# Kernel optimization log

Measured on AMD Instinct MI355X. Metric: run time of the kernel, lower is better.

The kernel has to match this reference:

```python
import jax, jax.numpy as jnp
import numpy as np

B, T, E, H, V, O = 64, 512, 128, 256, 100000, 1


def setup_inputs() -> dict:
    key = jax.random.key(0)
    ks = jax.random.split(key, 10)
    sE, sH = 1.0 / np.sqrt(E), 1.0 / np.sqrt(H)
    return {
        "x": jax.random.randint(ks[0], (B, T), 0, V),
        "emb_table": jax.random.normal(ks[1], (V, E), jnp.float32) * 0.1,
        "W_ih": jax.random.normal(ks[2], (4 * H, E), jnp.float32) * sE,  # torch gate order i,f,g,o
        "W_hh": jax.random.normal(ks[3], (4 * H, H), jnp.float32) * sH,
        "b_ih": jnp.zeros((4 * H,), jnp.float32),  # biases init'd to 0 in source
        "b_hh": jnp.zeros((4 * H,), jnp.float32),
        "Wm": jax.random.normal(ks[4], (H, H), jnp.float32) * sH,
        "bm": jnp.zeros((H,), jnp.float32),
        "Wf": jax.random.normal(ks[5], (O, H), jnp.float32) * sH,
        "bf": jnp.zeros((O,), jnp.float32),
    }


def reference(x, emb_table, W_ih, W_hh, b_ih, b_hh, Wm, bm, Wf, bf):
    batch = x.shape[0]
    hid = W_hh.shape[1]
    # vectorized replacement for the per-(i,j) python-loop embedding copy
    embeds = emb_table[x]                                  # [B,T,E]
    # precompute input contribution to all gates for every timestep
    gx = jnp.einsum('bte,ge->btg', embeds, W_ih) + b_ih     # [B,T,4H]
    gx = jnp.swapaxes(gx, 0, 1)                             # [T,B,4H]
    h0 = jnp.zeros((batch, hid), embeds.dtype)
    c0 = jnp.zeros((batch, hid), embeds.dtype)

    def step(carry, g_t):
        h, c = carry
        g = g_t + h @ W_hh.T + b_hh                         # [B,4H]
        i, f, gg, o = jnp.split(g, 4, axis=-1)
        i, f, o = jax.nn.sigmoid(i), jax.nn.sigmoid(f), jax.nn.sigmoid(o)
        c = f * c + i * jnp.tanh(gg)
        h = o * jnp.tanh(c)
        return (h, c), h

    (hT, cT), hs = jax.lax.scan(step, (h0, c0), gx)
    out = jnp.swapaxes(hs, 0, 1)                            # [B,T,H]
    out = out @ Wm.T + bm                                   # ffmiddle
    out = out @ Wf.T + bf                                   # fc -> [B,T,O]
    sig_out = jax.nn.sigmoid(out).reshape(batch, -1).mean(axis=1)  # [B]
    # hidden = (h_n, c_n) with leading num_layers=1 dim, as in torch
    return sig_out, hT[None, :, :], cT[None, :, :]
```

## Files before the change

kernel.cpp:

```cpp
#include <hip/hip_runtime.h>


#define BATCH 64
#define TSTEPS 512
#define EDIM 128
#define HDIM 256
#define G4H 1024

typedef short bf16x8 __attribute__((ext_vector_type(8)));
typedef short bf16x4 __attribute__((ext_vector_type(4)));
typedef float f32x4 __attribute__((ext_vector_type(4)));

__device__ __forceinline__ unsigned short f2bf(float f) {
  unsigned u = __builtin_bit_cast(unsigned, f);
  return (unsigned short)((u + 0x7fffu + ((u >> 16) & 1u)) >> 16);
}
__device__ __forceinline__ float bf2f(unsigned short h) {
  unsigned u = ((unsigned)h) << 16;
  return __builtin_bit_cast(float, u);
}
__device__ __forceinline__ unsigned pk2(float a, float b) {
  return (unsigned)f2bf(a) | ((unsigned)f2bf(b) << 16);
}
__device__ __forceinline__ float fsig(float x) {
  return __builtin_amdgcn_rcpf(1.f + __expf(-x));
}
__device__ __forceinline__ float ftanh(float x) {
  return 1.f - 2.f * __builtin_amdgcn_rcpf(__expf(2.f * x) + 1.f);
}
__device__ __forceinline__ bf16x8 ldfrag(const unsigned short* p) {
  bf16x4 a = *(const bf16x4*)p;
  bf16x4 b = *(const bf16x4*)(p + 16);
  return __builtin_shufflevector(a, b, 0, 1, 2, 3, 4, 5, 6, 7);
}
__device__ __forceinline__ bf16x8 pack8(float4 v0, float4 v1) {
  bf16x8 f;
  f[0] = (short)f2bf(v0.x); f[1] = (short)f2bf(v0.y);
  f[2] = (short)f2bf(v0.z); f[3] = (short)f2bf(v0.w);
  f[4] = (short)f2bf(v1.x); f[5] = (short)f2bf(v1.y);
  f[6] = (short)f2bf(v1.z); f[7] = (short)f2bf(v1.w);
  return f;
}

__global__ __launch_bounds__(256) void k_gx(const int* __restrict__ x,
                                            const float* __restrict__ emb,
                                            const float* __restrict__ Wih,
                                            const float* __restrict__ bih,
                                            unsigned short* __restrict__ gx3) {
  const int t = blockIdx.x;
  const int g0 = blockIdx.y * 64;
  const int tid = threadIdx.x;
  __shared__ unsigned short Al[64 * 136];
  __shared__ unsigned short Bl[64 * 136];
  __shared__ int tok[64];
  if (tid < 64) tok[tid] = x[tid * TSTEPS + t];
  __syncthreads();
  {
    const int r = tid >> 2, c0 = (tid & 3) * 32;
    const float* asrc = emb + (size_t)tok[r] * EDIM + c0;
    const float* bsrc = Wih + (size_t)(g0 + r) * EDIM + c0;
#pragma unroll
    for (int s = 0; s < 32; s += 8) {
      float4 a0 = *(const float4*)(asrc + s);
      float4 a1 = *(const float4*)(asrc + s + 4);
      uint4 pa = {pk2(a0.x, a0.y), pk2(a0.z, a0.w), pk2(a1.x, a1.y), pk2(a1.z, a1.w)};
      *(uint4*)&Al[r * 136 + c0 + s] = pa;
      float4 b0 = *(const float4*)(bsrc + s);
      float4 b1 = *(const float4*)(bsrc + s + 4);
      uint4 pb = {pk2(b0.x, b0.y), pk2(b0.z, b0.w), pk2(b1.x, b1.y), pk2(b1.z, b1.w)};
      *(uint4*)&Bl[r * 136 + c0 + s] = pb;
    }
  }
  __syncthreads();
  const int lane = tid & 63, w = tid >> 6;
  const int lo = lane & 15, hi = lane >> 4;
  const int mb = (w & 1) * 32, nb = (w >> 1) * 32;
  f32x4 acc[2][2];
#pragma unroll
  for (int jj = 0; jj < 2; ++jj) {
    float bv = bih[g0 + nb + jj * 16 + lo];
    acc[0][jj] = (f32x4){bv, bv, bv, bv};
    acc[1][jj] = acc[0][jj];
  }
#pragma unroll
  for (int kk = 0; kk < 4; ++kk) {
    bf16x8 af0 = ldfrag(&Al[(mb + lo) * 136 + kk * 32 + hi * 4]);
    bf16x8 af1 = ldfrag(&Al[(mb + 16 + lo) * 136 + kk * 32 + hi * 4]);
    bf16x8 bf0 = ldfrag(&Bl[(nb + lo) * 136 + kk * 32 + hi * 4]);
    bf16x8 bf1 = ldfrag(&Bl[(nb + 16 + lo) * 136 + kk * 32 + hi * 4]);
    acc[0][0] = __builtin_amdgcn_mfma_f32_16x16x32_bf16(af0, bf0, acc[0][0], 0, 0, 0);
    acc[0][1] = __builtin_amdgcn_mfma_f32_16x16x32_bf16(af0, bf1, acc[0][1], 0, 0, 0);
    acc[1][0] = __builtin_amdgcn_mfma_f32_16x16x32_bf16(af1, bf0, acc[1][0], 0, 0, 0);
    acc[1][1] = __builtin_amdgcn_mfma_f32_16x16x32_bf16(af1, bf1, acc[1][1], 0, 0, 0);
  }
#pragma unroll
  for (int i = 0; i < 2; ++i)
#pragma unroll
    for (int jj = 0; jj < 2; ++jj) {
      int grp = (w & 1) * 2 + i;
      int col = g0 + nb + jj * 16 + lo;
      int g = col >> 8, jc = col & 255;
      int halfb = jc >> 7, wv = (jc >> 4) & 7, lov = jc & 15;
      size_t base = (((size_t)(t * 8 + grp * 2 + halfb) * 8 + wv) * 64 +
                     (hi * 16 + lov)) * 16 + g * 4;
      unsigned long long val =
          (unsigned long long)pk2(acc[i][jj][0], acc[i][jj][1]) |
          ((unsigned long long)pk2(acc[i][jj][2], acc[i][jj][3]) << 32);
      *(unsigned long long*)&gx3[base] = val;
    }
}

__global__ __launch_bounds__(512, 2) void k_rec(const unsigned short* __restrict__ gx3,
                                                const float* __restrict__ Whh,
                                                const float* __restrict__ bhh,
                                                const float* __restrict__ weff,
                                                unsigned long long* __restrict__ hx,
                                                float* __restrict__ out) {
  const int tid = threadIdx.x;
  const int bp = blockIdx.x;
  const int grp = bp >> 1, half = bp & 1;
  const int b0 = grp * 16;
  const int lane = tid & 63, w = tid >> 6;
  const int lo = lane & 15, hi = lane >> 4;
  const int j = half * 128 + w * 16 + lo;
  __shared__ unsigned short h_lds[2][32 * 136];
  bf16x8 wf[4][8];
  float bhv[4];
#pragma unroll
  for (int g = 0; g < 4; ++g) {
    const float* wr = Whh + (size_t)(g * 256 + j) * HDIM;
    bhv[g] = bhh[g * 256 + j];
#pragma unroll
    for (int kk = 0; kk < 8; ++kk) {
      const float* p = wr + kk * 32 + hi * 8;
      wf[g][kk] = pack8(*(const float4*)p, *(const float4*)(p + 4));
    }
  }
  const int hb_b = tid >> 5, hb_g = tid & 31;
  float wv8[8];
#pragma unroll
  for (int e = 0; e < 8; ++e) wv8[e] = weff[hb_g * 8 + e];
  const float c0 = weff[256];
  float sig_acc = 0.f;
  for (int i = tid; i < 32 * 136 / 2; i += 512) ((unsigned*)h_lds[0])[i] = 0u;
  const unsigned short* gp = gx3 + (((size_t)bp * 8 + w) * 64 + lane) * 16;
  unsigned gwE[8], gwO[8];
  {
    uint4 a = *(const uint4*)(gp);
    uint4 b = *(const uint4*)(gp + 8);
    gwE[0] = a.x; gwE[1] = a.y; gwE[2] = a.z; gwE[3] = a.w;
    gwE[4] = b.x; gwE[5] = b.y; gwE[6] = b.z; gwE[7] = b.w;
    uint4 c2 = *(const uint4*)(gp + 65536);
    uint4 d2 = *(const uint4*)(gp + 65536 + 8);
    gwO[0] = c2.x; gwO[1] = c2.y; gwO[2] = c2.z; gwO[3] = c2.w;
    gwO[4] = d2.x; gwO[5] = d2.y; gwO[6] = d2.z; gwO[7] = d2.w;
  }
  float c[4] = {0.f, 0.f, 0.f, 0.f};
  float hv[4];
  f32x4 acc[4];
  const int ob = (j >> 3) * 136 + (j & 7);
  const int jp = ((half ^ 1) * 128) + ((tid >> 6) << 4) + (tid & 15);
  const int hip = (tid >> 4) & 3;
  const int pb = (jp >> 3) * 136 + (jp & 7);
  __syncthreads();

  auto cinit = [&](const unsigned (&G)[8]) {
#pragma unroll
    for (int g = 0; g < 4; ++g)
#pragma unroll
      for (int r = 0; r < 4; ++r) {
        unsigned word = G[g * 2 + (r >> 1)];
        unsigned short v = (r & 1) ? (unsigned short)(word >> 16) : (unsigned short)word;
        acc[g][r] = bf2f(v) + bhv[g];
      }
  };
  auto mfma_own = [&](int buf) {
    if (half == 0) {
#pragma unroll
      for (int kk = 0; kk < 4; ++kk) {
        bf16x8 a = *(const bf16x8*)&h_lds[buf][(kk * 4 + hi) * 136 + lo * 8];
#pragma unroll
        for (int g = 0; g < 4; ++g)
          acc[g] = __builtin_amdgcn_mfma_f32_16x16x32_bf16(a, wf[g][kk], acc[g], 0, 0, 0);
      }
    } else {
#pragma unroll
      for (int kk = 4; kk < 8; ++kk) {
        bf16x8 a = *(const bf16x8*)&h_lds[buf][(kk * 4 + hi) * 136 + lo * 8];
#pragma unroll
        for (int g = 0; g < 4; ++g)
          acc[g] = __builtin_amdgcn_mfma_f32_16x16x32_bf16(a, wf[g][kk], acc[g], 0, 0, 0);
      }
    }
  };
  auto mfma_par = [&](int buf) {
    if (half == 0) {
#pragma unroll
      for (int kk = 4; kk < 8; ++kk) {
        bf16x8 a = *(const bf16x8*)&h_lds[buf][(kk * 4 + hi) * 136 + lo * 8];
#pragma unroll
        for (int g = 0; g < 4; ++g)
          acc[g] = __builtin_amdgcn_mfma_f32_16x16x32_bf16(a, wf[g][kk], acc[g], 0, 0, 0);
      }
    } else {
#pragma unroll
      for (int kk = 0; kk < 4; ++kk) {
        bf16x8 a = *(const bf16x8*)&h_lds[buf][(kk * 4 + hi) * 136 + lo * 8];
#pragma unroll
        for (int g = 0; g < 4; ++g)
          acc[g] = __builtin_amdgcn_mfma_f32_16x16x32_bf16(a, wf[g][kk], acc[g], 0, 0, 0);
      }
    }
  };
  auto update_store = [&](int t) {
    const unsigned wt = (unsigned)(t + 1);
    unsigned short hbf[4];
#pragma unroll
    for (int r = 0; r < 4; ++r) {
      float iv = fsig(acc[0][r]), fv = fsig(acc[1][r]);
      float gv = ftanh(acc[2][r]), ov = fsig(acc[3][r]);
      c[r] = fv * c[r] + iv * gv;
      hv[r] = ov * ftanh(c[r]);
      hbf[r] = f2bf(hv[r]);
    }
    const int par = (int)(wt & 1u);
    unsigned long long* dst = &hx[((size_t)(par * 8 + bp)) * 1024 + w * 128 + lane * 2];
    const unsigned long long tg = ((unsigned long long)wt) << 32;
    __hip_atomic_store(&dst[0], tg | (unsigned long long)pk2(hv[0], hv[1]),
                       __ATOMIC_RELAXED, __HIP_MEMORY_SCOPE_AGENT);
    __hip_atomic_store(&dst[1], tg | (unsigned long long)pk2(hv[2], hv[3]),
                       __ATOMIC_RELAXED, __HIP_MEMORY_SCOPE_AGENT);
    asm volatile("" ::: "memory");
#pragma unroll
    for (int r = 0; r < 4; ++r) h_lds[par][ob + (hi * 4 + r) * 8] = hbf[r];
  };
  auto head = [&](int buf) {
    bf16x8 hh = *(const bf16x8*)&h_lds[buf][hb_g * 136 + hb_b * 8];
    float s = 0.f;
#pragma unroll
    for (int e = 0; e < 8; ++e) s += bf2f((unsigned short)hh[e]) * wv8[e];
    s += __shfl_xor(s, 1);  s += __shfl_xor(s, 2);  s += __shfl_xor(s, 4);
    s += __shfl_xor(s, 8);  s += __shfl_xor(s, 16);
    sig_acc += fsig(s + c0);
  };
  auto gx_issue = [&](int s, unsigned (&G)[8]) {
    const unsigned short* q = gp + (size_t)s * 65536;
    uint4 a = *(const uint4*)(q);
    uint4 b = *(const uint4*)(q + 8);
    G[0] = a.x; G[1] = a.y; G[2] = a.z; G[3] = a.w;
    G[4] = b.x; G[5] = b.y; G[6] = b.z; G[7] = b.w;
  };
  auto poll_write = [&](int t) {
    const unsigned wt = (unsigned)(t + 1);
    const int par = (int)(wt & 1u);
    unsigned long long* src = &hx[((size_t)(par * 8 + (bp ^ 1))) * 1024 + tid * 2];
    unsigned long long a0 = __hip_atomic_load(&src[0], __ATOMIC_RELAXED, __HIP_MEMORY_SCOPE_AGENT);
    unsigned long long a1 = __hip_atomic_load(&src[1], __ATOMIC_RELAXED, __HIP_MEMORY_SCOPE_AGENT);
    unsigned long long b0 = __hip_atomic_load(&src[0], __ATOMIC_RELAXED, __HIP_MEMORY_SCOPE_AGENT);
    unsigned long long b1 = __hip_atomic_load(&src[1], __ATOMIC_RELAXED, __HIP_MEMORY_SCOPE_AGENT);
    unsigned long long v0, v1;
    for (;;) {
      if ((unsigned)(a0 >> 32) == wt && (unsigned)(a1 >> 32) == wt) { v0 = a0; v1 = a1; break; }
      a0 = b0; a1 = b1;
      b0 = __hip_atomic_load(&src[0], __ATOMIC_RELAXED, __HIP_MEMORY_SCOPE_AGENT);
      b1 = __hip_atomic_load(&src[1], __ATOMIC_RELAXED, __HIP_MEMORY_SCOPE_AGENT);
    }
    h_lds[par][pb + (hip * 4 + 0) * 8] = (unsigned short)v0;
    h_lds[par][pb + (hip * 4 + 1) * 8] = (unsigned short)(v0 >> 16);
    h_lds[par][pb + (hip * 4 + 2) * 8] = (unsigned short)v1;
    h_lds[par][pb + (hip * 4 + 3) * 8] = (unsigned short)(v1 >> 16);
  };
  auto body = [&](int t, unsigned (&Gc)[8], unsigned (&Gf)[8]) {
    mfma_par(t & 1);
    update_store(t);
    if (t + 2 < TSTEPS) gx_issue(t + 2, Gf);
    __syncthreads();
    if (t < TSTEPS - 1) {
      cinit(Gc);
      mfma_own((t + 1) & 1);
    }
    head(t & 1);
    poll_write(t);
    __syncthreads();
  };

  cinit(gwE);
  update_store(0);
  gx_issue(2, gwE);
  __syncthreads();
  cinit(gwO);
  mfma_own(1);
  poll_write(0);
  __syncthreads();
  for (int t = 1; t + 1 < TSTEPS - 1; t += 2) {
    body(t, gwE, gwO);
    body(t + 1, gwO, gwE);
  }
  body(TSTEPS - 1, gwE, gwO);
  head(0);
  if (half == 0 && hb_g == 0) out[b0 + hb_b] = sig_acc * (1.f / 512.f);
#pragma unroll
  for (int r = 0; r < 4; ++r) {
    const int b = b0 + hi * 4 + r;
    out[64 + b * HDIM + j] = hv[r];
    out[64 + BATCH * HDIM + b * HDIM + j] = c[r];
  }
}

__global__ __launch_bounds__(256) void k_weff(const float* __restrict__ Wm,
                                              const float* __restrict__ bm,
                                              const float* __restrict__ Wf,
                                              const float* __restrict__ bfb,
                                              float* __restrict__ weff) {
  const int k = threadIdx.x;
  __shared__ float red[256];
  float acc = 0.f;
#pragma unroll 8
  for (int jj = 0; jj < 256; ++jj) acc += Wf[jj] * Wm[jj * 256 + k];
  weff[k] = acc;
  red[k] = bm[k] * Wf[k];
  __syncthreads();
  for (int s = 128; s > 0; s >>= 1) {
    if (k < s) red[k] += red[k + s];
    __syncthreads();
  }
  if (k == 0) weff[256] = red[0] + bfb[0];
}

extern "C" void kernel_launch(void* const* d_in, const int* in_sizes, int n_in,
                              void* d_out, int out_size, void* d_ws, size_t ws_size,
                              hipStream_t stream) {
  (void)in_sizes; (void)n_in; (void)out_size; (void)ws_size;
  const int* x = (const int*)d_in[0];
  const float* emb = (const float*)d_in[1];
  const float* Wih = (const float*)d_in[2];
  const float* Whh = (const float*)d_in[3];
  const float* bih = (const float*)d_in[4];
  const float* bhh = (const float*)d_in[5];
  const float* Wm  = (const float*)d_in[6];
  const float* bm  = (const float*)d_in[7];
  const float* Wf  = (const float*)d_in[8];
  const float* bf  = (const float*)d_in[9];
  float* out = (float*)d_out;
  char* ws = (char*)d_ws;
  const size_t gx_bytes = (size_t)TSTEPS * BATCH * G4H * 2;
  const size_t hx_bytes = (size_t)2 * 8 * 1024 * 8;
  unsigned short* gx3 = (unsigned short*)ws;
  unsigned long long* hx = (unsigned long long*)(ws + gx_bytes);
  float* weff = (float*)(ws + gx_bytes + hx_bytes);
  hipMemsetAsync(hx, 0, hx_bytes, stream);
  k_gx<<<dim3(512, 16), 256, 0, stream>>>(x, emb, Wih, bih, gx3);
  k_weff<<<1, 256, 0, stream>>>(Wm, bm, Wf, bf, weff);
  k_rec<<<8, 512, 0, stream>>>(gx3, Whh, bhh, weff, hx, out);
}
```

Baseline: 1.034 ms.

## Split exchange roles across warps and overlap peer polling with MFMA

Cross-block hidden-state exchange now uses a role split: warps 0-3 read packed h from LDS and publish it to global with four 64-bit tagged stores each, while warps 4-7 issue the peer loads before their own-half MFMAs and only spin and write to LDS afterward. The gx prefetch is also moved to the start of each step. The aim is to hide the latency of cross-CU polling behind compute and to use wider, coalesced transfers. The cost is warp imbalance and an extra LDS read before publishing, which adds latency to the critical path.

```diff
diff --git a/kernel.cpp b/kernel.cpp
--- a/kernel.cpp
+++ b/kernel.cpp
@@ -159,9 +159,8 @@
   float hv[4];
   f32x4 acc[4];
   const int ob = (j >> 3) * 136 + (j & 7);
-  const int jp = ((half ^ 1) * 128) + ((tid >> 6) << 4) + (tid & 15);
-  const int hip = (tid >> 4) & 3;
-  const int pb = (jp >> 3) * 136 + (jp & 7);
+  const int ogran = half * 16;
+  const int pgran = (half ^ 1) * 16;
   __syncthreads();
 
   auto cinit = [&](const unsigned (&G)[8]) {
@@ -212,8 +211,8 @@
       }
     }
   };
-  auto update_store = [&](int t) {
-    const unsigned wt = (unsigned)(t + 1);
+  auto update = [&](int t) {
+    const int par = (int)((t + 1) & 1u);
     unsigned short hbf[4];
 #pragma unroll
     for (int r = 0; r < 4; ++r) {
@@ -223,14 +222,6 @@
       hv[r] = ov * ftanh(c[r]);
       hbf[r] = f2bf(hv[r]);
     }
-    const int par = (int)(wt & 1u);
-    unsigned long long* dst = &hx[((size_t)(par * 8 + bp)) * 1024 + w * 128 + lane * 2];
-    const unsigned long long tg = ((unsigned long long)wt) << 32;
-    __hip_atomic_store(&dst[0], tg | (unsigned long long)pk2(hv[0], hv[1]),
-                       __ATOMIC_RELAXED, __HIP_MEMORY_SCOPE_AGENT);
-    __hip_atomic_store(&dst[1], tg | (unsigned long long)pk2(hv[2], hv[3]),
-                       __ATOMIC_RELAXED, __HIP_MEMORY_SCOPE_AGENT);
-    asm volatile("" ::: "memory");
 #pragma unroll
     for (int r = 0; r < 4; ++r) h_lds[par][ob + (hi * 4 + r) * 8] = hbf[r];
   };
@@ -250,47 +241,84 @@
     G[0] = a.x; G[1] = a.y; G[2] = a.z; G[3] = a.w;
     G[4] = b.x; G[5] = b.y; G[6] = b.z; G[7] = b.w;
   };
-  auto poll_write = [&](int t) {
+  auto xstore = [&](int t) {
     const unsigned wt = (unsigned)(t + 1);
     const int par = (int)(wt & 1u);
-    unsigned long long* src = &hx[((size_t)(par * 8 + (bp ^ 1))) * 1024 + tid * 2];
-    unsigned long long a0 = __hip_atomic_load(&src[0], __ATOMIC_RELAXED, __HIP_MEMORY_SCOPE_AGENT);
-    unsigned long long a1 = __hip_atomic_load(&src[1], __ATOMIC_RELAXED, __HIP_MEMORY_SCOPE_AGENT);
-    unsigned long long b0 = __hip_atomic_load(&src[0], __ATOMIC_RELAXED, __HIP_MEMORY_SCOPE_AGENT);
-    unsigned long long b1 = __hip_atomic_load(&src[1], __ATOMIC_RELAXED, __HIP_MEMORY_SCOPE_AGENT);
-    unsigned long long v0, v1;
-    for (;;) {
-      if ((unsigned)(a0 >> 32) == wt && (unsigned)(a1 >> 32) == wt) { v0 = a0; v1 = a1; break; }
-      a0 = b0; a1 = b1;
-      b0 = __hip_atomic_load(&src[0], __ATOMIC_RELAXED, __HIP_MEMORY_SCOPE_AGENT);
-      b1 = __hip_atomic_load(&src[1], __ATOMIC_RELAXED, __HIP_MEMORY_SCOPE_AGENT);
-    }
-    h_lds[par][pb + (hip * 4 + 0) * 8] = (unsigned short)v0;
-    h_lds[par][pb + (hip * 4 + 1) * 8] = (unsigned short)(v0 >> 16);
-    h_lds[par][pb + (hip * 4 + 2) * 8] = (unsigned short)v1;
-    h_lds[par][pb + (hip * 4 + 3) * 8] = (unsigned short)(v1 >> 16);
+    const int b = tid >> 4, g = tid & 15;
+    uint4 hc = *(const uint4*)&h_lds[par][(ogran + g) * 136 + b * 8];
+    const unsigned long long tg = ((unsigned long long)wt) << 32;
+    unsigned long long* dst = &hx[((size_t)(par * 8 + bp)) * 1024];
+    __hip_atomic_store(&dst[0 * 256 + tid], tg | (unsigned long long)hc.x,
+                       __ATOMIC_RELAXED, __HIP_MEMORY_SCOPE_AGENT);
+    __hip_atomic_store(&dst[1 * 256 + tid], tg | (unsigned long long)hc.y,
+                       __ATOMIC_RELAXED, __HIP_MEMORY_SCOPE_AGENT);
+    __hip_atomic_store(&dst[2 * 256 + tid], tg | (unsigned long long)hc.z,
+                       __ATOMIC_RELAXED, __HIP_MEMORY_SCOPE_AGENT);
+    __hip_atomic_store(&dst[3 * 256 + tid], tg | (unsigned long long)hc.w,
+                       __ATOMIC_RELAXED, __HIP_MEMORY_SCOPE_AGENT);
+    asm volatile("" ::: "memory");
+  };
+  auto pissue = [&](int t, unsigned long long (&A)[4]) {
+    const unsigned wt = (unsigned)(t + 1);
+    const int par = (int)(wt & 1u);
+    const int pid = tid - 256;
+    const unsigned long long* src = &hx[((size_t)(par * 8 + (bp ^ 1))) * 1024];
+    A[0] = __hip_atomic_load(&src[0 * 256 + pid], __ATOMIC_RELAXED, __HIP_MEMORY_SCOPE_AGENT);
+    A[1] = __hip_atomic_load(&src[1 * 256 + pid], __ATOMIC_RELAXED, __HIP_MEMORY_SCOPE_AGENT);
+    A[2] = __hip_atomic_load(&src[2 * 256 + pid], __ATOMIC_RELAXED, __HIP_MEMORY_SCOPE_AGENT);
+    A[3] = __hip_atomic_load(&src[3 * 256 + pid], __ATOMIC_RELAXED, __HIP_MEMORY_SCOPE_AGENT);
+    asm volatile("" ::: "memory");
+  };
+  auto pfinish = [&](int t, unsigned long long (&A)[4]) {
+    const unsigned wt = (unsigned)(t + 1);
+    const int par = (int)(wt & 1u);
+    const int pid = tid - 256;
+    const unsigned long long* src = &hx[((size_t)(par * 8 + (bp ^ 1))) * 1024];
+    while (!((unsigned)(A[0] >> 32) == wt && (unsigned)(A[1] >> 32) == wt &&
+             (unsigned)(A[2] >> 32) == wt && (unsigned)(A[3] >> 32) == wt)) {
+      A[0] = __hip_atomic_load(&src[0 * 256 + pid], __ATOMIC_RELAXED, __HIP_MEMORY_SCOPE_AGENT);
+      A[1] = __hip_atomic_load(&src[1 * 256 + pid], __ATOMIC_RELAXED, __HIP_MEMORY_SCOPE_AGENT);
+      A[2] = __hip_atomic_load(&src[2 * 256 + pid], __ATOMIC_RELAXED, __HIP_MEMORY_SCOPE_AGENT);
+      A[3] = __hip_atomic_load(&src[3 * 256 + pid], __ATOMIC_RELAXED, __HIP_MEMORY_SCOPE_AGENT);
+    }
+    const int b = pid >> 4, g = pid & 15;
+    *(uint4*)&h_lds[par][(pgran + g) * 136 + b * 8] =
+        (uint4){(unsigned)A[0], (unsigned)A[1], (unsigned)A[2], (unsigned)A[3]};
   };
   auto body = [&](int t, unsigned (&Gc)[8], unsigned (&Gf)[8]) {
+    if (t + 2 < TSTEPS) gx_issue(t + 2, Gf);
     mfma_par(t & 1);
-    update_store(t);
-    if (t + 2 < TSTEPS) gx_issue(t + 2, Gf);
+    update(t);
     __syncthreads();
-    if (t < TSTEPS - 1) {
-      cinit(Gc);
-      mfma_own((t + 1) & 1);
-    }
-    head(t & 1);
-    poll_write(t);
+    if (w < 4) {
+      xstore(t);
+      if (t < TSTEPS - 1) { cinit(Gc); mfma_own((t + 1) & 1); }
+      head(t & 1);
+    } else {
+      unsigned long long A[4];
+      pissue(t, A);
+      if (t < TSTEPS - 1) { cinit(Gc); mfma_own((t + 1) & 1); }
+      head(t & 1);
+      pfinish(t, A);
+    }
     __syncthreads();
   };
 
   cinit(gwE);
-  update_store(0);
+  update(0);
   gx_issue(2, gwE);
   __syncthreads();
-  cinit(gwO);
-  mfma_own(1);
-  poll_write(0);
+  if (w < 4) {
+    xstore(0);
+    cinit(gwO);
+    mfma_own(1);
+  } else {
+    unsigned long long A[4];
+    pissue(0, A);
+    cinit(gwO);
+    mfma_own(1);
+    pfinish(0, A);
+  }
   __syncthreads();
   for (int t = 1; t + 1 < TSTEPS - 1; t += 2) {
     body(t, gwE, gwO);
```

Result: slower. 1.406 ms (+35.9%).

## Split recurrence across 16 blocks with fast sc0 polling and fallback exchange path

Applied to the files above, without the earlier changes.

The recurrent kernel now runs 16 blocks, each pair owning 8 batch rows instead of 16, with half-tiles padded in the MFMA rows. Hidden-state exchange between paired blocks is written twice: once with sc0 cache-hint inline-asm stores polled by a bounded spin loop, and once via agent-scope atomics used as a fallback when the fast path times out. The gx prefetch is also moved ahead of the MFMA phase. The aim is to cut per-step exchange latency and spread the work over more CUs, at the cost of duplicated stores, wasted MFMA rows and reliance on the cache-hint path being coherent enough.

```diff
diff --git a/kernel.cpp b/kernel.cpp
--- a/kernel.cpp
+++ b/kernel.cpp
@@ -110,16 +110,18 @@
     }
 }
 
-__global__ __launch_bounds__(512, 2) void k_rec(const unsigned short* __restrict__ gx3,
+__global__ __launch_bounds__(512, 1) void k_rec(const unsigned short* __restrict__ gx3,
                                                 const float* __restrict__ Whh,
                                                 const float* __restrict__ bhh,
                                                 const float* __restrict__ weff,
-                                                unsigned long long* __restrict__ hx,
+                                                unsigned long long* __restrict__ hxA,
+                                                unsigned long long* __restrict__ hxB,
                                                 float* __restrict__ out) {
   const int tid = threadIdx.x;
   const int bp = blockIdx.x;
-  const int grp = bp >> 1, half = bp & 1;
-  const int b0 = grp * 16;
+  const int grp = bp & 7, half = bp >> 3;
+  const int s = grp & 1;
+  const int slot = (grp >> 1) * 2 + half;
   const int lane = tid & 63, w = tid >> 6;
   const int lo = lane & 15, hi = lane >> 4;
   const int j = half * 128 + w * 16 + lo;
@@ -143,7 +145,8 @@
   const float c0 = weff[256];
   float sig_acc = 0.f;
   for (int i = tid; i < 32 * 136 / 2; i += 512) ((unsigned*)h_lds[0])[i] = 0u;
-  const unsigned short* gp = gx3 + (((size_t)bp * 8 + w) * 64 + lane) * 16;
+  const int glane = (s * 2 + (hi & 1)) * 16 + lo;
+  const unsigned short* gp = gx3 + (((size_t)slot * 8 + w) * 64 + glane) * 16;
   unsigned gwE[8], gwO[8];
   {
     uint4 a = *(const uint4*)(gp);
@@ -162,6 +165,7 @@
   const int jp = ((half ^ 1) * 128) + ((tid >> 6) << 4) + (tid & 15);
   const int hip = (tid >> 4) & 3;
   const int pb = (jp >> 3) * 136 + (jp & 7);
+  bool fast = true;
   __syncthreads();
 
   auto cinit = [&](const unsigned (&G)[8]) {
@@ -212,8 +216,8 @@
       }
     }
   };
-  auto update_store = [&](int t) {
-    const unsigned wt = (unsigned)(t + 1);
+  auto update = [&](int t) {
+    const int par = (int)((t + 1) & 1u);
     unsigned short hbf[4];
 #pragma unroll
     for (int r = 0; r < 4; ++r) {
@@ -223,74 +227,103 @@
       hv[r] = ov * ftanh(c[r]);
       hbf[r] = f2bf(hv[r]);
     }
-    const int par = (int)(wt & 1u);
-    unsigned long long* dst = &hx[((size_t)(par * 8 + bp)) * 1024 + w * 128 + lane * 2];
+    const unsigned wt = (unsigned)(t + 1);
     const unsigned long long tg = ((unsigned long long)wt) << 32;
-    __hip_atomic_store(&dst[0], tg | (unsigned long long)pk2(hv[0], hv[1]),
-                       __ATOMIC_RELAXED, __HIP_MEMORY_SCOPE_AGENT);
-    __hip_atomic_store(&dst[1], tg | (unsigned long long)pk2(hv[2], hv[3]),
-                       __ATOMIC_RELAXED, __HIP_MEMORY_SCOPE_AGENT);
-    asm volatile("" ::: "memory");
+    const unsigned long long d0 = tg | (unsigned long long)pk2(hv[0], hv[1]);
+    const unsigned long long d1 = tg | (unsigned long long)pk2(hv[2], hv[3]);
+    {
+      unsigned long long dstA = (unsigned long long)
+          (hxA + ((size_t)(par * 16 + bp)) * 1024 + w * 128 + lane * 2);
+      asm volatile("global_store_dwordx2 %0, %1, off sc0\n\t"
+                   "global_store_dwordx2 %0, %2, off offset:8 sc0"
+                   :: "v"(dstA), "v"(d0), "v"(d1) : "memory");
+      unsigned long long* dstB = hxB + ((size_t)(par * 16 + bp)) * 1024 + w * 128 + lane * 2;
+      __hip_atomic_store(&dstB[0], d0, __ATOMIC_RELAXED, __HIP_MEMORY_SCOPE_AGENT);
+      __hip_atomic_store(&dstB[1], d1, __ATOMIC_RELAXED, __HIP_MEMORY_SCOPE_AGENT);
+      asm volatile("" ::: "memory");
+    }
 #pragma unroll
     for (int r = 0; r < 4; ++r) h_lds[par][ob + (hi * 4 + r) * 8] = hbf[r];
   };
   auto head = [&](int buf) {
     bf16x8 hh = *(const bf16x8*)&h_lds[buf][hb_g * 136 + hb_b * 8];
-    float s = 0.f;
-#pragma unroll
-    for (int e = 0; e < 8; ++e) s += bf2f((unsigned short)hh[e]) * wv8[e];
-    s += __shfl_xor(s, 1);  s += __shfl_xor(s, 2);  s += __shfl_xor(s, 4);
-    s += __shfl_xor(s, 8);  s += __shfl_xor(s, 16);
-    sig_acc += fsig(s + c0);
-  };
-  auto gx_issue = [&](int s, unsigned (&G)[8]) {
-    const unsigned short* q = gp + (size_t)s * 65536;
+    float sv = 0.f;
+#pragma unroll
+    for (int e = 0; e < 8; ++e) sv += bf2f((unsigned short)hh[e]) * wv8[e];
+    sv += __shfl_xor(sv, 1);  sv += __shfl_xor(sv, 2);  sv += __shfl_xor(sv, 4);
+    sv += __shfl_xor(sv, 8);  sv += __shfl_xor(sv, 16);
+    sig_acc += fsig(sv + c0);
+  };
+  auto gx_issue = [&](int st, unsigned (&G)[8]) {
+    const unsigned short* q = gp + (size_t)st * 65536;
     uint4 a = *(const uint4*)(q);
     uint4 b = *(const uint4*)(q + 8);
     G[0] = a.x; G[1] = a.y; G[2] = a.z; G[3] = a.w;
     G[4] = b.x; G[5] = b.y; G[6] = b.z; G[7] = b.w;
   };
-  auto poll_write = [&](int t) {
+  auto pollB = [&](int t, unsigned long long& v0, unsigned long long& v1) {
     const unsigned wt = (unsigned)(t + 1);
     const int par = (int)(wt & 1u);
-    unsigned long long* src = &hx[((size_t)(par * 8 + (bp ^ 1))) * 1024 + tid * 2];
-    unsigned long long a0 = __hip_atomic_load(&src[0], __ATOMIC_RELAXED, __HIP_MEMORY_SCOPE_AGENT);
-    unsigned long long a1 = __hip_atomic_load(&src[1], __ATOMIC_RELAXED, __HIP_MEMORY_SCOPE_AGENT);
-    unsigned long long b0 = __hip_atomic_load(&src[0], __ATOMIC_RELAXED, __HIP_MEMORY_SCOPE_AGENT);
-    unsigned long long b1 = __hip_atomic_load(&src[1], __ATOMIC_RELAXED, __HIP_MEMORY_SCOPE_AGENT);
-    unsigned long long v0, v1;
-    for (;;) {
-      if ((unsigned)(a0 >> 32) == wt && (unsigned)(a1 >> 32) == wt) { v0 = a0; v1 = a1; break; }
-      a0 = b0; a1 = b1;
-      b0 = __hip_atomic_load(&src[0], __ATOMIC_RELAXED, __HIP_MEMORY_SCOPE_AGENT);
-      b1 = __hip_atomic_load(&src[1], __ATOMIC_RELAXED, __HIP_MEMORY_SCOPE_AGENT);
-    }
+    unsigned long long* src = hxB + ((size_t)(par * 16 + (bp ^ 8))) * 1024 + tid * 2;
+    do {
+      v0 = __hip_atomic_load(&src[0], __ATOMIC_RELAXED, __HIP_MEMORY_SCOPE_AGENT);
+      v1 = __hip_atomic_load(&src[1], __ATOMIC_RELAXED, __HIP_MEMORY_SCOPE_AGENT);
+    } while ((unsigned)(v0 >> 32) != wt || (unsigned)(v1 >> 32) != wt);
+  };
+  auto poll = [&](int t, unsigned long long& v0, unsigned long long& v1) {
+    const unsigned wt = (unsigned)(t + 1);
+    const int par = (int)(wt & 1u);
+    if (fast) {
+      const unsigned long long srcA = (unsigned long long)
+          (hxA + ((size_t)(par * 16 + (bp ^ 8))) * 1024 + tid * 2);
+      bool done = false;
+      unsigned long long a0 = 0, a1 = 0;
+      for (int k2 = 0; k2 < 24 && __any(!done); ++k2) {
+        unsigned long long s0, s1;
+        asm volatile("global_load_dwordx2 %0, %2, off sc0\n\t"
+                     "global_load_dwordx2 %1, %2, off offset:8 sc0\n\t"
+                     "s_waitcnt vmcnt(0)"
+                     : "=&v"(s0), "=&v"(s1) : "v"(srcA) : "memory");
+        if (!done && (unsigned)(s0 >> 32) == wt && (unsigned)(s1 >> 32) == wt) {
+          a0 = s0; a1 = s1; done = true;
+        }
+      }
+      if (__any(!done)) fast = false;
+      else { v0 = a0; v1 = a1; return; }
+    }
+    pollB(t, v0, v1);
+  };
+  auto pwrite = [&](int t, unsigned long long v0, unsigned long long v1) {
+    const int par = (int)((t + 1) & 1u);
     h_lds[par][pb + (hip * 4 + 0) * 8] = (unsigned short)v0;
     h_lds[par][pb + (hip * 4 + 1) * 8] = (unsigned short)(v0 >> 16);
     h_lds[par][pb + (hip * 4 + 2) * 8] = (unsigned short)v1;
     h_lds[par][pb + (hip * 4 + 3) * 8] = (unsigned short)(v1 >> 16);
   };
   auto body = [&](int t, unsigned (&Gc)[8], unsigned (&Gf)[8]) {
+    if (t + 2 < TSTEPS) gx_issue(t + 2, Gf);
     mfma_par(t & 1);
-    update_store(t);
-    if (t + 2 < TSTEPS) gx_issue(t + 2, Gf);
+    update(t);
     __syncthreads();
-    if (t < TSTEPS - 1) {
-      cinit(Gc);
-      mfma_own((t + 1) & 1);
-    }
+    if (t < TSTEPS - 1) { cinit(Gc); mfma_own((t + 1) & 1); }
     head(t & 1);
-    poll_write(t);
+    unsigned long long v0, v1;
+    poll(t, v0, v1);
+    pwrite(t, v0, v1);
     __syncthreads();
   };
 
   cinit(gwE);
-  update_store(0);
+  update(0);
   gx_issue(2, gwE);
   __syncthreads();
   cinit(gwO);
   mfma_own(1);
-  poll_write(0);
+  {
+    unsigned long long v0, v1;
+    pollB(0, v0, v1);
+    pwrite(0, v0, v1);
+  }
   __syncthreads();
   for (int t = 1; t + 1 < TSTEPS - 1; t += 2) {
     body(t, gwE, gwO);
@@ -298,12 +331,14 @@
   }
   body(TSTEPS - 1, gwE, gwO);
   head(0);
-  if (half == 0 && hb_g == 0) out[b0 + hb_b] = sig_acc * (1.f / 512.f);
-#pragma unroll
-  for (int r = 0; r < 4; ++r) {
-    const int b = b0 + hi * 4 + r;
-    out[64 + b * HDIM + j] = hv[r];
-    out[64 + BATCH * HDIM + b * HDIM + j] = c[r];
+  if (half == 0 && hb_g == 0 && hb_b < 8) out[grp * 8 + hb_b] = sig_acc * (1.f / 512.f);
+  if (hi < 2) {
+#pragma unroll
+    for (int r = 0; r < 4; ++r) {
+      const int b = grp * 8 + hi * 4 + r;
+      out[64 + b * HDIM + j] = hv[r];
+      out[64 + BATCH * HDIM + b * HDIM + j] = c[r];
+    }
   }
 }
 
@@ -320,8 +355,8 @@
   weff[k] = acc;
   red[k] = bm[k] * Wf[k];
   __syncthreads();
-  for (int s = 128; s > 0; s >>= 1) {
-    if (k < s) red[k] += red[k + s];
+  for (int sred = 128; sred > 0; sred >>= 1) {
+    if (k < sred) red[k] += red[k + sred];
     __syncthreads();
   }
   if (k == 0) weff[256] = red[0] + bfb[0];
@@ -344,12 +379,13 @@
   float* out = (float*)d_out;
   char* ws = (char*)d_ws;
   const size_t gx_bytes = (size_t)TSTEPS * BATCH * G4H * 2;
-  const size_t hx_bytes = (size_t)2 * 8 * 1024 * 8;
+  const size_t hx_set = (size_t)2 * 16 * 1024 * 8;
   unsigned short* gx3 = (unsigned short*)ws;
-  unsigned long long* hx = (unsigned long long*)(ws + gx_bytes);
-  float* weff = (float*)(ws + gx_bytes + hx_bytes);
-  hipMemsetAsync(hx, 0, hx_bytes, stream);
+  unsigned long long* hxA = (unsigned long long*)(ws + gx_bytes);
+  unsigned long long* hxB = (unsigned long long*)(ws + gx_bytes + hx_set);
+  float* weff = (float*)(ws + gx_bytes + 2 * hx_set);
+  hipMemsetAsync(hxA, 0, 2 * hx_set, stream);
   k_gx<<<dim3(512, 16), 256, 0, stream>>>(x, emb, Wih, bih, gx3);
   k_weff<<<1, 256, 0, stream>>>(Wm, bm, Wf, bf, weff);
-  k_rec<<<8, 512, 0, stream>>>(gx3, Whh, bhh, weff, hx, out);
-}
+  k_rec<<<16, 512, 0, stream>>>(gx3, Whh, bhh, weff, hxA, hxB, out);
+}
```

Result: slower. 1.360 ms (+31.5%).

## Process two batch groups per recurrent block, halving the grid to four blocks

Applied to the files above, without the earlier changes.

Each recurrent block now handles two 16-row batch groups (A and B) instead of one, so the grid shrinks from 8 to 4 blocks. The W_hh fragments held in registers are reused across both groups, and the two groups' MFMA, update and poll phases are interleaved to hide latency. The unrolled even/odd prologue is replaced with a single uniform time loop. The trade-off is twice the per-block work on the serial critical path and higher register and LDS use, while fewer blocks take part in the cross-block exchange.

```diff
diff --git a/kernel.cpp b/kernel.cpp
--- a/kernel.cpp
+++ b/kernel.cpp
@@ -118,12 +118,14 @@
                                                 float* __restrict__ out) {
   const int tid = threadIdx.x;
   const int bp = blockIdx.x;
-  const int grp = bp >> 1, half = bp & 1;
-  const int b0 = grp * 16;
+  const int gpair = bp >> 1, half = bp & 1;
+  const int gA = gpair * 2, gB = gA + 1;
+  const int b0A = gA * 16, b0B = gB * 16;
+  const int slotA = gA * 2 + half, slotB = gB * 2 + half;
   const int lane = tid & 63, w = tid >> 6;
   const int lo = lane & 15, hi = lane >> 4;
   const int j = half * 128 + w * 16 + lo;
-  __shared__ unsigned short h_lds[2][32 * 136];
+  __shared__ unsigned short h_lds[2][2][32 * 136];
   bf16x8 wf[4][8];
   float bhv[4];
 #pragma unroll
@@ -141,30 +143,30 @@
 #pragma unroll
   for (int e = 0; e < 8; ++e) wv8[e] = weff[hb_g * 8 + e];
   const float c0 = weff[256];
-  float sig_acc = 0.f;
-  for (int i = tid; i < 32 * 136 / 2; i += 512) ((unsigned*)h_lds[0])[i] = 0u;
-  const unsigned short* gp = gx3 + (((size_t)bp * 8 + w) * 64 + lane) * 16;
-  unsigned gwE[8], gwO[8];
-  {
-    uint4 a = *(const uint4*)(gp);
-    uint4 b = *(const uint4*)(gp + 8);
-    gwE[0] = a.x; gwE[1] = a.y; gwE[2] = a.z; gwE[3] = a.w;
-    gwE[4] = b.x; gwE[5] = b.y; gwE[6] = b.z; gwE[7] = b.w;
-    uint4 c2 = *(const uint4*)(gp + 65536);
-    uint4 d2 = *(const uint4*)(gp + 65536 + 8);
-    gwO[0] = c2.x; gwO[1] = c2.y; gwO[2] = c2.z; gwO[3] = c2.w;
-    gwO[4] = d2.x; gwO[5] = d2.y; gwO[6] = d2.z; gwO[7] = d2.w;
-  }
-  float c[4] = {0.f, 0.f, 0.f, 0.f};
-  float hv[4];
-  f32x4 acc[4];
+  float sigA = 0.f, sigB = 0.f;
+  for (int i = tid; i < 32 * 136 / 2; i += 512) {
+    ((unsigned*)h_lds[0][0])[i] = 0u;
+    ((unsigned*)h_lds[1][0])[i] = 0u;
+  }
+  const unsigned short* gpA = gx3 + (((size_t)slotA * 8 + w) * 64 + lane) * 16;
+  const unsigned short* gpB = gx3 + (((size_t)slotB * 8 + w) * 64 + lane) * 16;
+  float cA[4] = {0.f, 0.f, 0.f, 0.f}, cB[4] = {0.f, 0.f, 0.f, 0.f};
+  float hvA[4], hvB[4];
+  f32x4 accA[4], accB[4];
+  unsigned GA[8], GB[8];
   const int ob = (j >> 3) * 136 + (j & 7);
   const int jp = ((half ^ 1) * 128) + ((tid >> 6) << 4) + (tid & 15);
   const int hip = (tid >> 4) & 3;
   const int pb = (jp >> 3) * 136 + (jp & 7);
-  __syncthreads();
-
-  auto cinit = [&](const unsigned (&G)[8]) {
+
+  auto gx_issue = [&](const unsigned short* gp, int st, unsigned (&G)[8]) {
+    const unsigned short* q = gp + (size_t)st * 65536;
+    uint4 a = *(const uint4*)(q);
+    uint4 b = *(const uint4*)(q + 8);
+    G[0] = a.x; G[1] = a.y; G[2] = a.z; G[3] = a.w;
+    G[4] = b.x; G[5] = b.y; G[6] = b.z; G[7] = b.w;
+  };
+  auto cinit = [&](f32x4 (&acc)[4], const unsigned (&G)[8]) {
 #pragma unroll
     for (int g = 0; g < 4; ++g)
 #pragma unroll
@@ -174,11 +176,11 @@
         acc[g][r] = bf2f(v) + bhv[g];
       }
   };
-  auto mfma_own = [&](int buf) {
+  auto mfma_own = [&](f32x4 (&acc)[4], const unsigned short* hbuf) {
     if (half == 0) {
 #pragma unroll
       for (int kk = 0; kk < 4; ++kk) {
-        bf16x8 a = *(const bf16x8*)&h_lds[buf][(kk * 4 + hi) * 136 + lo * 8];
+        bf16x8 a = *(const bf16x8*)&hbuf[(kk * 4 + hi) * 136 + lo * 8];
 #pragma unroll
         for (int g = 0; g < 4; ++g)
           acc[g] = __builtin_amdgcn_mfma_f32_16x16x32_bf16(a, wf[g][kk], acc[g], 0, 0, 0);
@@ -186,18 +188,18 @@
     } else {
 #pragma unroll
       for (int kk = 4; kk < 8; ++kk) {
-        bf16x8 a = *(const bf16x8*)&h_lds[buf][(kk * 4 + hi) * 136 + lo * 8];
+        bf16x8 a = *(const bf16x8*)&hbuf[(kk * 4 + hi) * 136 + lo * 8];
 #pragma unroll
         for (int g = 0; g < 4; ++g)
           acc[g] = __builtin_amdgcn_mfma_f32_16x16x32_bf16(a, wf[g][kk], acc[g], 0, 0, 0);
       }
     }
   };
-  auto mfma_par = [&](int buf) {
+  auto mfma_par = [&](f32x4 (&acc)[4], const unsigned short* hbuf) {
     if (half == 0) {
 #pragma unroll
       for (int kk = 4; kk < 8; ++kk) {
-        bf16x8 a = *(const bf16x8*)&h_lds[buf][(kk * 4 + hi) * 136 + lo * 8];
+        bf16x8 a = *(const bf16x8*)&hbuf[(kk * 4 + hi) * 136 + lo * 8];
 #pragma unroll
         for (int g = 0; g < 4; ++g)
           acc[g] = __builtin_amdgcn_mfma_f32_16x16x32_bf16(a, wf[g][kk], acc[g], 0, 0, 0);
@@ -205,14 +207,15 @@
     } else {
 #pragma unroll
       for (int kk = 0; kk < 4; ++kk) {
-        bf16x8 a = *(const bf16x8*)&h_lds[buf][(kk * 4 + hi) * 136 + lo * 8];
+        bf16x8 a = *(const bf16x8*)&hbuf[(kk * 4 + hi) * 136 + lo * 8];
 #pragma unroll
         for (int g = 0; g < 4; ++g)
           acc[g] = __builtin_amdgcn_mfma_f32_16x16x32_bf16(a, wf[g][kk], acc[g], 0, 0, 0);
       }
     }
   };
-  auto update_store = [&](int t) {
+  auto upd = [&](int t, f32x4 (&acc)[4], float (&c)[4], float (&hv)[4],
+                 int slot, unsigned short* ldsNxt) {
     const unsigned wt = (unsigned)(t + 1);
     unsigned short hbf[4];
 #pragma unroll
@@ -224,7 +227,7 @@
       hbf[r] = f2bf(hv[r]);
     }
     const int par = (int)(wt & 1u);
-    unsigned long long* dst = &hx[((size_t)(par * 8 + bp)) * 1024 + w * 128 + lane * 2];
+    unsigned long long* dst = &hx[((size_t)(par * 8 + slot)) * 1024 + w * 128 + lane * 2];
     const unsigned long long tg = ((unsigned long long)wt) << 32;
     __hip_atomic_store(&dst[0], tg | (unsigned long long)pk2(hv[0], hv[1]),
                        __ATOMIC_RELAXED, __HIP_MEMORY_SCOPE_AGENT);
@@ -232,28 +235,21 @@
                        __ATOMIC_RELAXED, __HIP_MEMORY_SCOPE_AGENT);
     asm volatile("" ::: "memory");
 #pragma unroll
-    for (int r = 0; r < 4; ++r) h_lds[par][ob + (hi * 4 + r) * 8] = hbf[r];
-  };
-  auto head = [&](int buf) {
-    bf16x8 hh = *(const bf16x8*)&h_lds[buf][hb_g * 136 + hb_b * 8];
+    for (int r = 0; r < 4; ++r) ldsNxt[ob + (hi * 4 + r) * 8] = hbf[r];
+  };
+  auto head = [&](const unsigned short* hbuf, float& sig) {
+    bf16x8 hh = *(const bf16x8*)&hbuf[hb_g * 136 + hb_b * 8];
     float s = 0.f;
 #pragma unroll
     for (int e = 0; e < 8; ++e) s += bf2f((unsigned short)hh[e]) * wv8[e];
     s += __shfl_xor(s, 1);  s += __shfl_xor(s, 2);  s += __shfl_xor(s, 4);
     s += __shfl_xor(s, 8);  s += __shfl_xor(s, 16);
-    sig_acc += fsig(s + c0);
-  };
-  auto gx_issue = [&](int s, unsigned (&G)[8]) {
-    const unsigned short* q = gp + (size_t)s * 65536;
-    uint4 a = *(const uint4*)(q);
-    uint4 b = *(const uint4*)(q + 8);
-    G[0] = a.x; G[1] = a.y; G[2] = a.z; G[3] = a.w;
-    G[4] = b.x; G[5] = b.y; G[6] = b.z; G[7] = b.w;
-  };
-  auto poll_write = [&](int t) {
+    sig += fsig(s + c0);
+  };
+  auto pollw = [&](int t, int pslot, unsigned short* ldsNxt) {
     const unsigned wt = (unsigned)(t + 1);
     const int par = (int)(wt & 1u);
-    unsigned long long* src = &hx[((size_t)(par * 8 + (bp ^ 1))) * 1024 + tid * 2];
+    unsigned long long* src = &hx[((size_t)(par * 8 + pslot)) * 1024 + tid * 2];
     unsigned long long a0 = __hip_atomic_load(&src[0], __ATOMIC_RELAXED, __HIP_MEMORY_SCOPE_AGENT);
     unsigned long long a1 = __hip_atomic_load(&src[1], __ATOMIC_RELAXED, __HIP_MEMORY_SCOPE_AGENT);
     unsigned long long b0 = __hip_atomic_load(&src[0], __ATOMIC_RELAXED, __HIP_MEMORY_SCOPE_AGENT);
@@ -265,45 +261,53 @@
       b0 = __hip_atomic_load(&src[0], __ATOMIC_RELAXED, __HIP_MEMORY_SCOPE_AGENT);
       b1 = __hip_atomic_load(&src[1], __ATOMIC_RELAXED, __HIP_MEMORY_SCOPE_AGENT);
     }
-    h_lds[par][pb + (hip * 4 + 0) * 8] = (unsigned short)v0;
-    h_lds[par][pb + (hip * 4 + 1) * 8] = (unsigned short)(v0 >> 16);
-    h_lds[par][pb + (hip * 4 + 2) * 8] = (unsigned short)v1;
-    h_lds[par][pb + (hip * 4 + 3) * 8] = (unsigned short)(v1 >> 16);
-  };
-  auto body = [&](int t, unsigned (&Gc)[8], unsigned (&Gf)[8]) {
-    mfma_par(t & 1);
-    update_store(t);
-    if (t + 2 < TSTEPS) gx_issue(t + 2, Gf);
+    ldsNxt[pb + (hip * 4 + 0) * 8] = (unsigned short)v0;
+    ldsNxt[pb + (hip * 4 + 1) * 8] = (unsigned short)(v0 >> 16);
+    ldsNxt[pb + (hip * 4 + 2) * 8] = (unsigned short)v1;
+    ldsNxt[pb + (hip * 4 + 3) * 8] = (unsigned short)(v1 >> 16);
+  };
+
+  gx_issue(gpA, 0, GA);
+  gx_issue(gpB, 0, GB);
+  cinit(accA, GA);
+  cinit(accB, GB);
+  __syncthreads();
+  for (int t = 0; t < TSTEPS; ++t) {
+    const int cur = t & 1, nxt = cur ^ 1;
+    if (t + 1 < TSTEPS) { gx_issue(gpA, t + 1, GA); gx_issue(gpB, t + 1, GB); }
+    mfma_par(accA, &h_lds[0][cur][0]);
+    upd(t, accA, cA, hvA, slotA, &h_lds[0][nxt][0]);
+    mfma_par(accB, &h_lds[1][cur][0]);
+    upd(t, accB, cB, hvB, slotB, &h_lds[1][nxt][0]);
     __syncthreads();
     if (t < TSTEPS - 1) {
-      cinit(Gc);
-      mfma_own((t + 1) & 1);
-    }
-    head(t & 1);
-    poll_write(t);
+      cinit(accA, GA);
+      mfma_own(accA, &h_lds[0][nxt][0]);
+      cinit(accB, GB);
+      mfma_own(accB, &h_lds[1][nxt][0]);
+    }
+    if (t > 0) {
+      head(&h_lds[0][cur][0], sigA);
+      head(&h_lds[1][cur][0], sigB);
+    }
+    pollw(t, slotA ^ 1, &h_lds[0][nxt][0]);
+    pollw(t, slotB ^ 1, &h_lds[1][nxt][0]);
     __syncthreads();
-  };
-
-  cinit(gwE);
-  update_store(0);
-  gx_issue(2, gwE);
-  __syncthreads();
-  cinit(gwO);
-  mfma_own(1);
-  poll_write(0);
-  __syncthreads();
-  for (int t = 1; t + 1 < TSTEPS - 1; t += 2) {
-    body(t, gwE, gwO);
-    body(t + 1, gwO, gwE);
-  }
-  body(TSTEPS - 1, gwE, gwO);
-  head(0);
-  if (half == 0 && hb_g == 0) out[b0 + hb_b] = sig_acc * (1.f / 512.f);
+  }
+  head(&h_lds[0][0][0], sigA);
+  head(&h_lds[1][0][0], sigB);
+  if (half == 0 && hb_g == 0) {
+    out[b0A + hb_b] = sigA * (1.f / 512.f);
+    out[b0B + hb_b] = sigB * (1.f / 512.f);
+  }
 #pragma unroll
   for (int r = 0; r < 4; ++r) {
-    const int b = b0 + hi * 4 + r;
-    out[64 + b * HDIM + j] = hv[r];
-    out[64 + BATCH * HDIM + b * HDIM + j] = c[r];
+    const int bA = b0A + hi * 4 + r;
+    const int bB = b0B + hi * 4 + r;
+    out[64 + bA * HDIM + j] = hvA[r];
+    out[64 + BATCH * HDIM + bA * HDIM + j] = cA[r];
+    out[64 + bB * HDIM + j] = hvB[r];
+    out[64 + BATCH * HDIM + bB * HDIM + j] = cB[r];
   }
 }
 
@@ -351,5 +355,5 @@
   hipMemsetAsync(hx, 0, hx_bytes, stream);
   k_gx<<<dim3(512, 16), 256, 0, stream>>>(x, emb, Wih, bih, gx3);
   k_weff<<<1, 256, 0, stream>>>(Wm, bm, Wf, bf, weff);
-  k_rec<<<8, 512, 0, stream>>>(gx3, Whh, bhh, weff, hx, out);
-}
+  k_rec<<<4, 512, 0, stream>>>(gx3, Whh, bhh, weff, hx, out);
+}
```

Result: slower. 2.029 ms (+96.1%).
